# Performance work log

Measured on AMD Instinct MI355X. Metric: run time of the kernel, lower is better.

## Reference

```python
import jax, jax.numpy as jnp
import numpy as np

DIM = 768
HEADS = 12
HEAD_DIM = DIM // HEADS
B, N = 8, 1024


def setup_inputs() -> dict:
    key = jax.random.key(0)
    ks = jax.random.split(key, 5)
    x = jax.random.normal(ks[0], (B, N, DIM), dtype=jnp.float32)
    shared_rel_pos = jax.random.normal(ks[1], (HEADS, N, N), dtype=jnp.float32)
    qkv_w = jax.random.normal(ks[2], (3 * DIM, DIM), dtype=jnp.float32) * (DIM ** -0.5)
    proj_w = jax.random.normal(ks[3], (DIM, DIM), dtype=jnp.float32) * (DIM ** -0.5)
    proj_b = jnp.zeros((DIM,), dtype=jnp.float32)
    return {"x": x, "shared_rel_pos": shared_rel_pos, "qkv_w": qkv_w,
            "proj_w": proj_w, "proj_b": proj_b}


def reference(x, shared_rel_pos, qkv_w, proj_w, proj_b):
    Bt, Nt, C = x.shape
    scale = HEAD_DIM ** -0.5
    # qkv: Linear(dim, 3*dim, bias=False) -> (B, N, 3, H, hd) -> (3, B, H, N, hd)
    qkv = jnp.einsum('bnc,oc->bno', x, qkv_w)
    qkv = qkv.reshape(Bt, Nt, 3, HEADS, HEAD_DIM).transpose(2, 0, 3, 1, 4)
    q, k, v = qkv[0], qkv[1], qkv[2]
    # scaled dot-product attention with shared relative-position bias
    attn = jnp.einsum('bhqd,bhkd->bhqk', q, k) * scale
    attn = attn + shared_rel_pos[None]  # broadcast over batch
    attn = jax.nn.softmax(attn, axis=-1)
    out = jnp.einsum('bhqk,bhkd->bhqd', attn, v)
    out = out.transpose(0, 2, 1, 3).reshape(Bt, Nt, C)
    return jnp.einsum('bnc,oc->bno', out, proj_w) + proj_b
```

## Files before the change

### kernel.cpp

```cpp
#include <hip/hip_runtime.h>
#include <hip/hip_bf16.h>
#include <stdint.h>

#define HEADS 12
#define HD 64
#define SEQ 1024
#define CDIM 768
#define LOG2E 1.44269504f

typedef __attribute__((ext_vector_type(8))) short bfrag;
typedef __attribute__((ext_vector_type(4))) float facc;
typedef __attribute__((ext_vector_type(4))) _Float16 h4;
typedef __attribute__((ext_vector_type(2))) __fp16 pk2;

__device__ __forceinline__ ushort f2bf(float f) {
    union { float f; uint32_t u; } v; v.f = f;
    uint32_t u = v.u;
    uint32_t r = (u + 0x7FFFu + ((u >> 16) & 1u)) >> 16;
    return (ushort)r;
}
__device__ __forceinline__ ushort f2h(float f) {
    union { _Float16 h; ushort u; } c; c.h = (_Float16)f; return c.u;
}
__device__ __forceinline__ float h2f(uint32_t u16) {
    union { _Float16 h; ushort u; } c; c.u = (ushort)u16; return (float)c.h;
}
__device__ __forceinline__ h4 pack4h(float p0, float p1, float p2, float p3) {
    union { h4 v4; pk2 v2[2]; } u;
    u.v2[0] = __builtin_amdgcn_cvt_pkrtz(p0, p1);
    u.v2[1] = __builtin_amdgcn_cvt_pkrtz(p2, p3);
    return u.v4;
}
__device__ __forceinline__ float exp2_raw(float x) {
    float r;
    asm("v_exp_f32 %0, %1" : "=v"(r) : "v"(x));
    return r;
}

__global__ void cvt_all(const float* __restrict__ x, const float* __restrict__ qw,
                        const float* __restrict__ pw,
                        ushort* __restrict__ xd, ushort* __restrict__ qd,
                        ushort* __restrict__ pd) {
    long i = ((long)blockIdx.x * 256 + threadIdx.x) * 4;
    if (i < 6291456) {
        float4 v = *(const float4*)(x + i);
        ushort4 o = {f2bf(v.x), f2bf(v.y), f2bf(v.z), f2bf(v.w)};
        *(ushort4*)(xd + i) = o;
    } else if (i < 8060928) {
        long j = i - 6291456;
        float4 v = *(const float4*)(qw + j);
        ushort4 o = {f2bf(v.x), f2bf(v.y), f2bf(v.z), f2bf(v.w)};
        *(ushort4*)(qd + j) = o;
    } else if (i < 8650752) {
        long j = i - 8060928;
        float4 v = *(const float4*)(pw + j);
        ushort4 o = {f2bf(v.x), f2bf(v.y), f2bf(v.z), f2bf(v.w)};
        *(ushort4*)(pd + j) = o;
    }
}

#define GLOAD16(gsrc, ldst) \
    __builtin_amdgcn_global_load_lds((const __attribute__((address_space(1))) uint32_t*)(gsrc), \
                                     (__attribute__((address_space(3))) uint32_t*)(ldst), 16, 0, 0)

template<int EPI>
__global__ __launch_bounds__(256) void gemm_nt(
    const ushort* __restrict__ A, const ushort* __restrict__ Bm,
    ushort* __restrict__ qb, ushort* __restrict__ kb, ushort* __restrict__ vb,
    const float* __restrict__ projb, float* __restrict__ out,
    const float* __restrict__ relf, ushort* __restrict__ biash)
{
    __shared__ ushort As[128 * 64];
    __shared__ ushort Bs[128 * 64];
    const int t = threadIdx.x;

    int m0, o0;
    if (EPI == 0) {
        if (blockIdx.y < 4) {
            const int cb = blockIdx.y * 64 + blockIdx.x;
#pragma unroll 4
            for (int s = 0; s < 48; ++s) {
                long i = (((long)s * 256 + cb) * 256 + t) * 4;
                float4 v = *(const float4*)(relf + i);
                ushort4 o = {f2h(v.x * LOG2E), f2h(v.y * LOG2E),
                             f2h(v.z * LOG2E), f2h(v.w * LOG2E)};
                *(ushort4*)(biash + i) = o;
            }
            return;
        }
        m0 = blockIdx.x * 128;
        o0 = (blockIdx.y - 4) * 128;
    } else {
        m0 = blockIdx.x * 128;
        o0 = blockIdx.y * 128;
    }

    const int w = t >> 6, l = t & 63;
    const int wm = w >> 1, wn = w & 1;
    const int lr = l & 15, lg = l >> 4;

    facc acc[4][4] = {};

    const int srow = w * 8 + (l >> 3);
    const int sgr  = ((l & 7) ^ (l >> 3)) * 8;
    const ushort* Ag = A + (size_t)(m0 + srow) * CDIM + sgr;
    const ushort* Bg = Bm + (size_t)(o0 + srow) * CDIM + sgr;
    const int ldst = w * 512 + l * 8;

    for (int k0 = 0; k0 < CDIM; k0 += 64) {
        __syncthreads();
#pragma unroll
        for (int j = 0; j < 4; ++j) {
            GLOAD16(Ag + (size_t)(j * 32) * CDIM + k0, As + j * 2048 + ldst);
            GLOAD16(Bg + (size_t)(j * 32) * CDIM + k0, Bs + j * 2048 + ldst);
        }
        __syncthreads();
#pragma unroll
        for (int s = 0; s < 2; ++s) {
            bfrag af[4], bf[4];
            const int rg = ((s * 4 + lg) ^ (lr & 7)) * 8;
#pragma unroll
            for (int m = 0; m < 4; ++m)
                af[m] = *(const bfrag*)&As[(wm * 64 + m * 16 + lr) * 64 + rg];
#pragma unroll
            for (int n = 0; n < 4; ++n)
                bf[n] = *(const bfrag*)&Bs[(wn * 64 + n * 16 + lr) * 64 + rg];
#pragma unroll
            for (int m = 0; m < 4; ++m)
#pragma unroll
                for (int n = 0; n < 4; ++n)
                    acc[m][n] = __builtin_amdgcn_mfma_f32_16x16x32_bf16(af[m], bf[n], acc[m][n], 0, 0, 0);
        }
    }

    if (EPI == 0) {
        const int tsel = o0 / CDIM;
        const int h_base = (o0 % CDIM) / 64;
        if (tsel == 2) {
#pragma unroll
            for (int m = 0; m < 4; ++m) {
                int grow = m0 + wm * 64 + m * 16 + lg * 4;
                int b = grow >> 10, nn = grow & 1023;
#pragma unroll
                for (int n = 0; n < 4; ++n) {
                    int h = h_base + wn;
                    int d = n * 16 + lr;
                    ushort4 pk = {f2h(acc[m][n][0]), f2h(acc[m][n][1]),
                                  f2h(acc[m][n][2]), f2h(acc[m][n][3])};
                    *(ushort4*)&vb[(((size_t)(b * HEADS + h)) * 64 + d) * 1024 + nn] = pk;
                }
            }
        } else {
            ushort* dst = (tsel == 0) ? qb : kb;
            const float scl = (tsel == 0) ? 0.18033688f : 1.0f;
#pragma unroll
            for (int m = 0; m < 4; ++m) {
                int grow = m0 + wm * 64 + m * 16 + lg * 4;
#pragma unroll
                for (int n = 0; n < 4; ++n) {
                    int h = h_base + wn;
                    int d = n * 16 + lr;
#pragma unroll
                    for (int r = 0; r < 4; ++r) {
                        int row = grow + r;
                        int b = row >> 10, nn = row & 1023;
                        dst[(((size_t)(b * HEADS + h)) * SEQ + nn) * HD + d] = f2bf(acc[m][n][r] * scl);
                    }
                }
            }
        }
    } else {
#pragma unroll
        for (int m = 0; m < 4; ++m) {
            int grow = m0 + wm * 64 + m * 16 + lg * 4;
#pragma unroll
            for (int n = 0; n < 4; ++n) {
                int o = o0 + wn * 64 + n * 16 + lr;
                float bias = projb[o];
#pragma unroll
                for (int r = 0; r < 4; ++r)
                    out[(size_t)(grow + r) * CDIM + o] = acc[m][n][r] + bias;
            }
        }
    }
}

__global__ __launch_bounds__(256, 3) void attn_kernel(
    const ushort* __restrict__ qbuf, const ushort* __restrict__ kbuf,
    const ushort* __restrict__ vtbuf, const ushort* __restrict__ biash,
    ushort* __restrict__ attn_out)
{
    __shared__ ushort Ks[2][64 * 64];
    __shared__ ushort Vt[2][64 * 64];

    const int t = threadIdx.x;
    const int w = t >> 6, l = t & 63;
    const int lr = l & 15, lg = l >> 4;

    const int bid = blockIdx.x;
    const int lid = (bid & 7) * 96 + (bid >> 3);
    const int h  = lid >> 6;
    const int qt = (lid >> 3) & 7;
    const int b  = lid & 7;

    const int q0 = qt * 128;
    const size_t headoff = (size_t)(b * HEADS + h) * SEQ * HD;
    const int qrb = q0 + w * 32;

    bfrag aQ[2][2];
#pragma unroll
    for (int n = 0; n < 2; ++n) {
        const ushort* Qp = qbuf + headoff + (size_t)(qrb + n * 16 + lr) * HD;
        aQ[n][0] = *(const bfrag*)(Qp + lg * 8);
        aQ[n][1] = *(const bfrag*)(Qp + 32 + lg * 8);
    }

    float mrun[2] = {-1e30f, -1e30f};
    float lrun[2] = {0.0f, 0.0f};
    facc Ov[2][4] = {};

    const ushort* bprow[2];
#pragma unroll
    for (int n = 0; n < 2; ++n)
        bprow[n] = biash + ((size_t)h * SEQ + qrb + n * 16 + lr) * SEQ;

    const ushort* kbh  = kbuf  + headoff;
    const ushort* vtbh = vtbuf + (size_t)(b * HEADS + h) * 65536;
    const int srow = (w << 3) + (l >> 3);
    const int sgr  = ((l & 7) ^ (srow & 7)) << 3;

    const int g0 = (lg ^ (lr & 7)) << 3;

    GLOAD16(kbh + (size_t)srow * 64 + sgr,            &Ks[0][w * 512]);
    GLOAD16(kbh + (size_t)(srow + 32) * 64 + sgr,     &Ks[0][2048 + w * 512]);
    GLOAD16(vtbh + (size_t)srow * 1024 + sgr,         &Vt[0][w * 512]);
    GLOAD16(vtbh + (size_t)(srow + 32) * 1024 + sgr,  &Vt[0][2048 + w * 512]);
    uint2 bcur[2][4];
#pragma unroll
    for (int n = 0; n < 2; ++n)
#pragma unroll
        for (int c = 0; c < 4; ++c)
            bcur[n][c] = *(const uint2*)(bprow[n] + c * 16 + lg * 4);
    __syncthreads();

    for (int tt = 0; tt < 16; ++tt) {
        const int cur = tt & 1;
        const ushort* Kc = Ks[cur];
        const ushort* Vc = Vt[cur];

        if (tt < 15) {
            const int kvn = (tt + 1) << 6;
            GLOAD16(kbh + (size_t)(kvn + srow) * 64 + sgr,           &Ks[cur ^ 1][w * 512]);
            GLOAD16(kbh + (size_t)(kvn + srow + 32) * 64 + sgr,      &Ks[cur ^ 1][2048 + w * 512]);
            GLOAD16(vtbh + (size_t)srow * 1024 + kvn + sgr,          &Vt[cur ^ 1][w * 512]);
            GLOAD16(vtbh + (size_t)(srow + 32) * 1024 + kvn + sgr,   &Vt[cur ^ 1][2048 + w * 512]);
        }

        facc St[2][4];
        h4 pf[2][4];
        float psum[2] = {0.0f, 0.0f};
        float pmax[2] = {-3.0e38f, -3.0e38f};
#pragma unroll
        for (int c = 0; c < 4; ++c) {
            bfrag kf0 = *(const bfrag*)&Kc[(c * 16 + lr) * 64 + g0];
            bfrag kf1 = *(const bfrag*)&Kc[(c * 16 + lr) * 64 + (g0 ^ 32)];
#pragma unroll
            for (int n = 0; n < 2; ++n) {
                uint2 bb = bcur[n][c];
                facc s;
                s[0] = h2f(bb.x & 0xffffu);
                s[1] = h2f(bb.x >> 16);
                s[2] = h2f(bb.y & 0xffffu);
                s[3] = h2f(bb.y >> 16);
                s = __builtin_amdgcn_mfma_f32_16x16x32_bf16(kf0, aQ[n][0], s, 0, 0, 0);
                s = __builtin_amdgcn_mfma_f32_16x16x32_bf16(kf1, aQ[n][1], s, 0, 0, 0);
                St[n][c] = s;
                float p0 = exp2_raw(s[0] - mrun[n]);
                float p1 = exp2_raw(s[1] - mrun[n]);
                float p2f = exp2_raw(s[2] - mrun[n]);
                float p3 = exp2_raw(s[3] - mrun[n]);
                psum[n] += (p0 + p1) + (p2f + p3);
                pmax[n] = fmaxf(pmax[n], fmaxf(fmaxf(s[0], s[1]), fmaxf(s[2], s[3])));
                pf[n][c] = pack4h(p0, p1, p2f, p3);
            }
        }

        if (tt < 15) {
            const int kvn = (tt + 1) << 6;
#pragma unroll
            for (int n = 0; n < 2; ++n)
#pragma unroll
                for (int c = 0; c < 4; ++c)
                    bcur[n][c] = *(const uint2*)(bprow[n] + kvn + c * 16 + lg * 4);
        }

        int viol = (pmax[0] > mrun[0] + 14.0f) || (pmax[1] > mrun[1] + 14.0f);
        if (__any(viol)) {
#pragma unroll
            for (int n = 0; n < 2; ++n) {
                float pm = pmax[n];
                pm = fmaxf(pm, __shfl_xor(pm, 16));
                pm = fmaxf(pm, __shfl_xor(pm, 32));
                float mnew = fmaxf(mrun[n], pm);
                float al = exp2_raw(mrun[n] - mnew);
                psum[n] = 0.0f;
#pragma unroll
                for (int c = 0; c < 4; ++c) {
                    float p0 = exp2_raw(St[n][c][0] - mnew);
                    float p1 = exp2_raw(St[n][c][1] - mnew);
                    float p2f = exp2_raw(St[n][c][2] - mnew);
                    float p3 = exp2_raw(St[n][c][3] - mnew);
                    psum[n] += (p0 + p1) + (p2f + p3);
                    pf[n][c] = pack4h(p0, p1, p2f, p3);
                }
#pragma unroll
                for (int r = 0; r < 4; ++r) {
                    float a = __shfl(al, lg * 4 + r);
#pragma unroll
                    for (int d = 0; d < 4; ++d) Ov[n][d][r] *= a;
                }
                lrun[n] *= al;
                mrun[n] = mnew;
            }
        }

        __builtin_amdgcn_s_setprio(1);
#pragma unroll
        for (int c = 0; c < 4; ++c) {
#pragma unroll
            for (int d0 = 0; d0 < 4; ++d0) {
                int row = d0 * 16 + lr;
                h4 bv = *(const h4*)&Vc[row * 64 + ((((c * 2 + (lg >> 1)) ^ (lr & 7)) << 3) + ((lg & 1) << 2))];
#pragma unroll
                for (int n = 0; n < 2; ++n)
                    Ov[n][d0] = __builtin_amdgcn_mfma_f32_16x16x16f16(pf[n][c], bv, Ov[n][d0], 0, 0, 0);
            }
        }
        __builtin_amdgcn_s_setprio(0);

        lrun[0] += psum[0];
        lrun[1] += psum[1];

        if (tt < 15) __syncthreads();
    }

#pragma unroll
    for (int n = 0; n < 2; ++n) {
        float lt = lrun[n];
        lt += __shfl_xor(lt, 16);
        lt += __shfl_xor(lt, 32);
        ushort* op = attn_out + ((size_t)b * SEQ + qrb + n * 16) * CDIM + h * HD;
#pragma unroll
        for (int r = 0; r < 4; ++r) {
            float ll = __shfl(lt, lg * 4 + r);
            float rl = 1.0f / ll;
#pragma unroll
            for (int d = 0; d < 4; ++d)
                op[(size_t)(lg * 4 + r) * CDIM + d * 16 + lr] = f2bf(Ov[n][d][r] * rl);
        }
    }
}

extern "C" void kernel_launch(void* const* d_in, const int* in_sizes, int n_in,
                              void* d_out, int out_size, void* d_ws, size_t ws_size,
                              hipStream_t stream) {
    const float* x     = (const float*)d_in[0];
    const float* rel   = (const float*)d_in[1];
    const float* qkvw  = (const float*)d_in[2];
    const float* projw = (const float*)d_in[3];
    const float* projb = (const float*)d_in[4];
    float* out = (float*)d_out;

    char* ws = (char*)d_ws;
    ushort* biash = (ushort*)(ws);
    ushort* qb    = (ushort*)(ws + 25165824);
    ushort* kb    = (ushort*)(ws + 37748736);
    ushort* vb    = (ushort*)(ws + 50331648);
    ushort* attnb = (ushort*)(ws + 62914560);
    ushort* xbf   = attnb;
    ushort* wbf   = (ushort*)(ws + 75497472);
    ushort* pwbf  = (ushort*)(ws + 79036416);

    cvt_all<<<8448, 256, 0, stream>>>(x, qkvw, projw, xbf, wbf, pwbf);

    gemm_nt<0><<<dim3(64, 22), 256, 0, stream>>>(xbf, wbf, qb, kb, vb, nullptr, nullptr, rel, biash);
    attn_kernel<<<768, 256, 0, stream>>>(qb, kb, vb, biash, attnb);
    gemm_nt<1><<<dim3(64, 6), 256, 0, stream>>>(attnb, pwbf, nullptr, nullptr, nullptr, projb, out, nullptr, nullptr);
}
```

Baseline: 137.7 us.

## Peel first KV tile and fuse per-chunk exp with PV MFMA

Peels the first KV tile so the running max starts from the true max of the first block instead of a sentinel. In the remaining tiles, each 16-column chunk's probabilities are fed straight into the PV MFMAs, so the full S tile and P fragments no longer need to stay live. When the max threshold is exceeded, the block is no longer recomputed; only the accumulator and row sum are rescaled afterwards. This cuts register pressure and interleaves exp work with the PV matrix ops. The trade-off is that fp16 probabilities computed against a stale max can grow large, close to the fp16 limit, when scores jump sharply.

```diff
diff --git a/kernel.cpp b/kernel.cpp
--- a/kernel.cpp
+++ b/kernel.cpp
@@ -215,8 +215,8 @@
         aQ[n][1] = *(const bfrag*)(Qp + 32 + lg * 8);
     }
 
-    float mrun[2] = {-1e30f, -1e30f};
-    float lrun[2] = {0.0f, 0.0f};
+    float mrun[2];
+    float lrun[2];
     facc Ov[2][4] = {};
 
     const ushort* bprow[2];
@@ -243,27 +243,18 @@
             bcur[n][c] = *(const uint2*)(bprow[n] + c * 16 + lg * 4);
     __syncthreads();
 
-    for (int tt = 0; tt < 16; ++tt) {
-        const int cur = tt & 1;
-        const ushort* Kc = Ks[cur];
-        const ushort* Vc = Vt[cur];
-
-        if (tt < 15) {
-            const int kvn = (tt + 1) << 6;
-            GLOAD16(kbh + (size_t)(kvn + srow) * 64 + sgr,           &Ks[cur ^ 1][w * 512]);
-            GLOAD16(kbh + (size_t)(kvn + srow + 32) * 64 + sgr,      &Ks[cur ^ 1][2048 + w * 512]);
-            GLOAD16(vtbh + (size_t)srow * 1024 + kvn + sgr,          &Vt[cur ^ 1][w * 512]);
-            GLOAD16(vtbh + (size_t)(srow + 32) * 1024 + kvn + sgr,   &Vt[cur ^ 1][2048 + w * 512]);
-        }
+    {
+        GLOAD16(kbh + (size_t)(64 + srow) * 64 + sgr,            &Ks[1][w * 512]);
+        GLOAD16(kbh + (size_t)(64 + srow + 32) * 64 + sgr,       &Ks[1][2048 + w * 512]);
+        GLOAD16(vtbh + (size_t)srow * 1024 + 64 + sgr,           &Vt[1][w * 512]);
+        GLOAD16(vtbh + (size_t)(srow + 32) * 1024 + 64 + sgr,    &Vt[1][2048 + w * 512]);
 
         facc St[2][4];
-        h4 pf[2][4];
-        float psum[2] = {0.0f, 0.0f};
         float pmax[2] = {-3.0e38f, -3.0e38f};
 #pragma unroll
         for (int c = 0; c < 4; ++c) {
-            bfrag kf0 = *(const bfrag*)&Kc[(c * 16 + lr) * 64 + g0];
-            bfrag kf1 = *(const bfrag*)&Kc[(c * 16 + lr) * 64 + (g0 ^ 32)];
+            bfrag kf0 = *(const bfrag*)&Ks[0][(c * 16 + lr) * 64 + g0];
+            bfrag kf1 = *(const bfrag*)&Ks[0][(c * 16 + lr) * 64 + (g0 ^ 32)];
 #pragma unroll
             for (int n = 0; n < 2; ++n) {
                 uint2 bb = bcur[n][c];
@@ -275,13 +266,95 @@
                 s = __builtin_amdgcn_mfma_f32_16x16x32_bf16(kf0, aQ[n][0], s, 0, 0, 0);
                 s = __builtin_amdgcn_mfma_f32_16x16x32_bf16(kf1, aQ[n][1], s, 0, 0, 0);
                 St[n][c] = s;
+                pmax[n] = fmaxf(pmax[n], fmaxf(fmaxf(s[0], s[1]), fmaxf(s[2], s[3])));
+            }
+        }
+#pragma unroll
+        for (int n = 0; n < 2; ++n)
+#pragma unroll
+            for (int c = 0; c < 4; ++c)
+                bcur[n][c] = *(const uint2*)(bprow[n] + 64 + c * 16 + lg * 4);
+
+        h4 pf[2][4];
+#pragma unroll
+        for (int n = 0; n < 2; ++n) {
+            float pm = pmax[n];
+            pm = fmaxf(pm, __shfl_xor(pm, 16));
+            pm = fmaxf(pm, __shfl_xor(pm, 32));
+            mrun[n] = pm;
+            float sum = 0.0f;
+#pragma unroll
+            for (int c = 0; c < 4; ++c) {
+                float p0 = exp2_raw(St[n][c][0] - pm);
+                float p1 = exp2_raw(St[n][c][1] - pm);
+                float p2f = exp2_raw(St[n][c][2] - pm);
+                float p3 = exp2_raw(St[n][c][3] - pm);
+                sum += (p0 + p1) + (p2f + p3);
+                pf[n][c] = pack4h(p0, p1, p2f, p3);
+            }
+            lrun[n] = sum;
+        }
+        __builtin_amdgcn_s_setprio(1);
+#pragma unroll
+        for (int c = 0; c < 4; ++c) {
+#pragma unroll
+            for (int d0 = 0; d0 < 4; ++d0) {
+                int row = d0 * 16 + lr;
+                h4 bv = *(const h4*)&Vt[0][row * 64 + ((((c * 2 + (lg >> 1)) ^ (lr & 7)) << 3) + ((lg & 1) << 2))];
+#pragma unroll
+                for (int n = 0; n < 2; ++n)
+                    Ov[n][d0] = __builtin_amdgcn_mfma_f32_16x16x16f16(pf[n][c], bv, Ov[n][d0], 0, 0, 0);
+            }
+        }
+        __builtin_amdgcn_s_setprio(0);
+        __syncthreads();
+    }
+
+    for (int tt = 1; tt < 16; ++tt) {
+        const int cur = tt & 1;
+        const ushort* Kc = Ks[cur];
+        const ushort* Vc = Vt[cur];
+
+        if (tt < 15) {
+            const int kvn = (tt + 1) << 6;
+            GLOAD16(kbh + (size_t)(kvn + srow) * 64 + sgr,           &Ks[cur ^ 1][w * 512]);
+            GLOAD16(kbh + (size_t)(kvn + srow + 32) * 64 + sgr,      &Ks[cur ^ 1][2048 + w * 512]);
+            GLOAD16(vtbh + (size_t)srow * 1024 + kvn + sgr,          &Vt[cur ^ 1][w * 512]);
+            GLOAD16(vtbh + (size_t)(srow + 32) * 1024 + kvn + sgr,   &Vt[cur ^ 1][2048 + w * 512]);
+        }
+
+        float psum[2] = {0.0f, 0.0f};
+        float pmax[2] = {-3.0e38f, -3.0e38f};
+#pragma unroll
+        for (int c = 0; c < 4; ++c) {
+            bfrag kf0 = *(const bfrag*)&Kc[(c * 16 + lr) * 64 + g0];
+            bfrag kf1 = *(const bfrag*)&Kc[(c * 16 + lr) * 64 + (g0 ^ 32)];
+            h4 pf[2];
+#pragma unroll
+            for (int n = 0; n < 2; ++n) {
+                uint2 bb = bcur[n][c];
+                facc s;
+                s[0] = h2f(bb.x & 0xffffu);
+                s[1] = h2f(bb.x >> 16);
+                s[2] = h2f(bb.y & 0xffffu);
+                s[3] = h2f(bb.y >> 16);
+                s = __builtin_amdgcn_mfma_f32_16x16x32_bf16(kf0, aQ[n][0], s, 0, 0, 0);
+                s = __builtin_amdgcn_mfma_f32_16x16x32_bf16(kf1, aQ[n][1], s, 0, 0, 0);
                 float p0 = exp2_raw(s[0] - mrun[n]);
                 float p1 = exp2_raw(s[1] - mrun[n]);
                 float p2f = exp2_raw(s[2] - mrun[n]);
                 float p3 = exp2_raw(s[3] - mrun[n]);
                 psum[n] += (p0 + p1) + (p2f + p3);
                 pmax[n] = fmaxf(pmax[n], fmaxf(fmaxf(s[0], s[1]), fmaxf(s[2], s[3])));
-                pf[n][c] = pack4h(p0, p1, p2f, p3);
+                pf[n] = pack4h(p0, p1, p2f, p3);
+            }
+#pragma unroll
+            for (int d0 = 0; d0 < 4; ++d0) {
+                int row = d0 * 16 + lr;
+                h4 bv = *(const h4*)&Vc[row * 64 + ((((c * 2 + (lg >> 1)) ^ (lr & 7)) << 3) + ((lg & 1) << 2))];
+#pragma unroll
+                for (int n = 0; n < 2; ++n)
+                    Ov[n][d0] = __builtin_amdgcn_mfma_f32_16x16x16f16(pf[n], bv, Ov[n][d0], 0, 0, 0);
             }
         }
 
@@ -293,6 +366,9 @@
                 for (int c = 0; c < 4; ++c)
                     bcur[n][c] = *(const uint2*)(bprow[n] + kvn + c * 16 + lg * 4);
         }
+
+        lrun[0] += psum[0];
+        lrun[1] += psum[1];
 
         int viol = (pmax[0] > mrun[0] + 14.0f) || (pmax[1] > mrun[1] + 14.0f);
         if (__any(viol)) {
@@ -303,43 +379,16 @@
                 pm = fmaxf(pm, __shfl_xor(pm, 32));
                 float mnew = fmaxf(mrun[n], pm);
                 float al = exp2_raw(mrun[n] - mnew);
-                psum[n] = 0.0f;
-#pragma unroll
-                for (int c = 0; c < 4; ++c) {
-                    float p0 = exp2_raw(St[n][c][0] - mnew);
-                    float p1 = exp2_raw(St[n][c][1] - mnew);
-                    float p2f = exp2_raw(St[n][c][2] - mnew);
-                    float p3 = exp2_raw(St[n][c][3] - mnew);
-                    psum[n] += (p0 + p1) + (p2f + p3);
-                    pf[n][c] = pack4h(p0, p1, p2f, p3);
-                }
+                lrun[n] *= al;
 #pragma unroll
                 for (int r = 0; r < 4; ++r) {
                     float a = __shfl(al, lg * 4 + r);
 #pragma unroll
                     for (int d = 0; d < 4; ++d) Ov[n][d][r] *= a;
                 }
-                lrun[n] *= al;
                 mrun[n] = mnew;
             }
         }
-
-        __builtin_amdgcn_s_setprio(1);
-#pragma unroll
-        for (int c = 0; c < 4; ++c) {
-#pragma unroll
-            for (int d0 = 0; d0 < 4; ++d0) {
-                int row = d0 * 16 + lr;
-                h4 bv = *(const h4*)&Vc[row * 64 + ((((c * 2 + (lg >> 1)) ^ (lr & 7)) << 3) + ((lg & 1) << 2))];
-#pragma unroll
-                for (int n = 0; n < 2; ++n)
-                    Ov[n][d0] = __builtin_amdgcn_mfma_f32_16x16x16f16(pf[n][c], bv, Ov[n][d0], 0, 0, 0);
-            }
-        }
-        __builtin_amdgcn_s_setprio(0);
-
-        lrun[0] += psum[0];
-        lrun[1] += psum[1];
 
         if (tt < 15) __syncthreads();
     }
```

Result: no change. 140.4 us (+1.9%).

## Load K and V fragments directly from global memory instead of LDS staging

Applied to the files above, without the earlier changes.

Removes the double-buffered LDS staging of K and V tiles, along with the per-iteration barriers. Each wave now reads its MFMA operand fragments straight from global memory (through the caches). This drops the LDS traffic and the block-wide synchronisation, and frees LDS for occupancy. In exchange the four waves in a block each fetch the same K/V data redundantly from L1/L2, with no explicit prefetch to hide global latency.

```diff
diff --git a/kernel.cpp b/kernel.cpp
--- a/kernel.cpp
+++ b/kernel.cpp
@@ -190,9 +190,6 @@
     const ushort* __restrict__ vtbuf, const ushort* __restrict__ biash,
     ushort* __restrict__ attn_out)
 {
-    __shared__ ushort Ks[2][64 * 64];
-    __shared__ ushort Vt[2][64 * 64];
-
     const int t = threadIdx.x;
     const int w = t >> 6, l = t & 63;
     const int lr = l & 15, lg = l >> 4;
@@ -224,37 +221,19 @@
     for (int n = 0; n < 2; ++n)
         bprow[n] = biash + ((size_t)h * SEQ + qrb + n * 16 + lr) * SEQ;
 
-    const ushort* kbh  = kbuf  + headoff;
-    const ushort* vtbh = vtbuf + (size_t)(b * HEADS + h) * 65536;
-    const int srow = (w << 3) + (l >> 3);
-    const int sgr  = ((l & 7) ^ (srow & 7)) << 3;
-
-    const int g0 = (lg ^ (lr & 7)) << 3;
-
-    GLOAD16(kbh + (size_t)srow * 64 + sgr,            &Ks[0][w * 512]);
-    GLOAD16(kbh + (size_t)(srow + 32) * 64 + sgr,     &Ks[0][2048 + w * 512]);
-    GLOAD16(vtbh + (size_t)srow * 1024 + sgr,         &Vt[0][w * 512]);
-    GLOAD16(vtbh + (size_t)(srow + 32) * 1024 + sgr,  &Vt[0][2048 + w * 512]);
+    const ushort* kfp = kbuf + headoff + (size_t)lr * HD + lg * 8;
+    const ushort* vfp = vtbuf + (size_t)(b * HEADS + h) * 65536
+                      + (size_t)lr * 1024 + lg * 4;
+
     uint2 bcur[2][4];
 #pragma unroll
     for (int n = 0; n < 2; ++n)
 #pragma unroll
         for (int c = 0; c < 4; ++c)
             bcur[n][c] = *(const uint2*)(bprow[n] + c * 16 + lg * 4);
-    __syncthreads();
 
     for (int tt = 0; tt < 16; ++tt) {
-        const int cur = tt & 1;
-        const ushort* Kc = Ks[cur];
-        const ushort* Vc = Vt[cur];
-
-        if (tt < 15) {
-            const int kvn = (tt + 1) << 6;
-            GLOAD16(kbh + (size_t)(kvn + srow) * 64 + sgr,           &Ks[cur ^ 1][w * 512]);
-            GLOAD16(kbh + (size_t)(kvn + srow + 32) * 64 + sgr,      &Ks[cur ^ 1][2048 + w * 512]);
-            GLOAD16(vtbh + (size_t)srow * 1024 + kvn + sgr,          &Vt[cur ^ 1][w * 512]);
-            GLOAD16(vtbh + (size_t)(srow + 32) * 1024 + kvn + sgr,   &Vt[cur ^ 1][2048 + w * 512]);
-        }
+        const int kv0 = tt << 6;
 
         facc St[2][4];
         h4 pf[2][4];
@@ -262,8 +241,9 @@
         float pmax[2] = {-3.0e38f, -3.0e38f};
 #pragma unroll
         for (int c = 0; c < 4; ++c) {
-            bfrag kf0 = *(const bfrag*)&Kc[(c * 16 + lr) * 64 + g0];
-            bfrag kf1 = *(const bfrag*)&Kc[(c * 16 + lr) * 64 + (g0 ^ 32)];
+            const ushort* kp = kfp + (size_t)(kv0 + c * 16) * 64;
+            bfrag kf0 = *(const bfrag*)(kp);
+            bfrag kf1 = *(const bfrag*)(kp + 32);
 #pragma unroll
             for (int n = 0; n < 2; ++n) {
                 uint2 bb = bcur[n][c];
@@ -286,7 +266,7 @@
         }
 
         if (tt < 15) {
-            const int kvn = (tt + 1) << 6;
+            const int kvn = kv0 + 64;
 #pragma unroll
             for (int n = 0; n < 2; ++n)
 #pragma unroll
@@ -329,8 +309,7 @@
         for (int c = 0; c < 4; ++c) {
 #pragma unroll
             for (int d0 = 0; d0 < 4; ++d0) {
-                int row = d0 * 16 + lr;
-                h4 bv = *(const h4*)&Vc[row * 64 + ((((c * 2 + (lg >> 1)) ^ (lr & 7)) << 3) + ((lg & 1) << 2))];
+                h4 bv = *(const h4*)(vfp + (size_t)(d0 * 16) * 1024 + kv0 + c * 16);
 #pragma unroll
                 for (int n = 0; n < 2; ++n)
                     Ov[n][d0] = __builtin_amdgcn_mfma_f32_16x16x16f16(pf[n][c], bv, Ov[n][d0], 0, 0, 0);
@@ -340,8 +319,6 @@
 
         lrun[0] += psum[0];
         lrun[1] += psum[1];
-
-        if (tt < 15) __syncthreads();
     }
 
 #pragma unroll
```

After: 251.7 us. +82.8%, slower.
